# Performance work log

Hardware: AMD Instinct MI355X
Metric: run time of the kernel (lower is better)

Reference implementation:

```python
import jax, jax.numpy as jnp
import numpy as np

B, S, HID = 2, 1024, 4096
NH, NKV, HD = 32, 8, 128
GROUPS = NH // NKV  # 4
BITS = 8
SCALING = HD ** -0.5


def quantize_lastdim(x, bits=BITS):
    """Asymmetric min-max fake-quant per row of the last dim (groupsize=-1),
    matching ActQuantizer.find_params + quantize/dequantize."""
    qmax = float(2 ** bits - 1)
    xmin = jnp.minimum(jnp.min(x, axis=-1, keepdims=True), 0.0)
    xmax = jnp.maximum(jnp.max(x, axis=-1, keepdims=True), 0.0)
    rng = xmax - xmin
    scale = jnp.where(rng == 0, 1.0, rng / qmax)
    zero = jnp.round(-xmin / scale)
    q = jnp.clip(jnp.round(x / scale) + zero, 0.0, qmax)
    return (q - zero) * scale


def rotate_half(x):
    x1, x2 = jnp.split(x, 2, axis=-1)
    return jnp.concatenate([-x2, x1], axis=-1)


def setup_inputs() -> dict:
    key = jax.random.key(0)
    ks = jax.random.split(key, 5)
    hidden_states = jax.random.normal(ks[0], (B, S, HID), dtype=jnp.float32)
    w_std = 0.02
    Wq = w_std * jax.random.normal(ks[1], (NH * HD, HID), dtype=jnp.float32)
    Wk = w_std * jax.random.normal(ks[2], (NKV * HD, HID), dtype=jnp.float32)
    Wv = w_std * jax.random.normal(ks[3], (NKV * HD, HID), dtype=jnp.float32)
    Wo = w_std * jax.random.normal(ks[4], (HID, NH * HD), dtype=jnp.float32)
    # RoPE tables (theta=10000)
    inv_freq = 1.0 / (10000.0 ** (jnp.arange(0, HD, 2, dtype=jnp.float32) / HD))
    freqs = jnp.outer(jnp.arange(S, dtype=jnp.float32), inv_freq)  # [S, HD/2]
    emb = jnp.concatenate([freqs, freqs], axis=-1)  # [S, HD]
    cos = jnp.broadcast_to(jnp.cos(emb)[None], (B, S, HD)).astype(jnp.float32)
    sin = jnp.broadcast_to(jnp.sin(emb)[None], (B, S, HD)).astype(jnp.float32)
    # additive causal mask [B,1,S,S]
    causal = jnp.tril(jnp.ones((S, S), dtype=bool))
    attention_mask = jnp.where(causal, 0.0, -1e9).astype(jnp.float32)
    attention_mask = jnp.broadcast_to(attention_mask[None, None], (B, 1, S, S))
    return {"hidden_states": hidden_states, "cos": cos, "sin": sin,
            "attention_mask": attention_mask, "Wq": Wq, "Wk": Wk, "Wv": Wv, "Wo": Wo}


def reference(hidden_states, cos, sin, attention_mask, Wq, Wk, Wv, Wo):
    b, s, _ = hidden_states.shape
    # projections -> [B, H, S, D]
    q = (hidden_states @ Wq.T).reshape(b, s, NH, HD).transpose(0, 2, 1, 3)
    k = (hidden_states @ Wk.T).reshape(b, s, NKV, HD).transpose(0, 2, 1, 3)
    v = (hidden_states @ Wv.T).reshape(b, s, NKV, HD).transpose(0, 2, 1, 3)
    # RoPE (HF: unsqueeze cos/sin at head dim)
    c = cos[:, None, :, :]
    si = sin[:, None, :, :]
    q = q * c + rotate_half(q) * si
    k = k * c + rotate_half(k) * si
    # SmoothK per-channel: subtract per-channel mean over the sequence
    # (softmax-invariant outlier smoothing of K before quantization)
    k = k - jnp.mean(k, axis=2, keepdims=True)
    # activation fake-quant of Q, K (per token over head_dim)
    q = quantize_lastdim(q)
    k = quantize_lastdim(k)
    # V quantized along the sequence axis (module transposes dims 2,3 first)
    v = quantize_lastdim(v.transpose(0, 1, 3, 2)).transpose(0, 1, 3, 2)
    # GQA repeat
    k_rep = jnp.repeat(k, GROUPS, axis=1)
    v_rep = jnp.repeat(v, GROUPS, axis=1)
    scores = jnp.einsum('bhqd,bhkd->bhqk', q, k_rep) * SCALING + attention_mask
    w = jax.nn.softmax(scores.astype(jnp.float32), axis=-1).astype(q.dtype)
    # fake-quant attention weights per row (groupsize=-1, so no padding)
    w = quantize_lastdim(w)
    attn = jnp.einsum('bhqk,bhkd->bhqd', w, v_rep)
    attn = attn.transpose(0, 2, 1, 3).reshape(b, s, NH * HD)
    out = attn @ Wo.T
    return (out, w)
```

## Files before the change

### kernel.cpp

```cpp
#include <hip/hip_runtime.h>
#include <math.h>
#include <stdint.h>

typedef unsigned int u32;
typedef unsigned short u16;
typedef __bf16 bf16x8 __attribute__((ext_vector_type(8)));
typedef float f32x4 __attribute__((ext_vector_type(4)));
typedef unsigned short u16x8 __attribute__((ext_vector_type(8)));
typedef unsigned short u16x4 __attribute__((ext_vector_type(4)));

constexpr int   Bb  = 2;
constexpr int   Ss  = 1024;
constexpr int   HID = 4096;
constexpr int   NH  = 32;
constexpr int   NKV = 8;
constexpr int   HD  = 128;
constexpr float SCALING = 0.0883883476483184405501f;

enum { M_QKV = 0, M_OUT = 3 };

__device__ __forceinline__ u16 f2bf(float f) {
  u32 u = __builtin_bit_cast(u32, f);
  u = u + 0x7fffu + ((u >> 16) & 1u);
  return (u16)(u >> 16);
}

__device__ __forceinline__ void gld_lds16(const void* g, void* l) {
  __builtin_amdgcn_global_load_lds(
      (const __attribute__((address_space(1))) u32*)(uintptr_t)g,
      (__attribute__((address_space(3))) u32*)(uintptr_t)l, 16, 0, 0);
}

template <int MODE, int NREP>
__global__ __launch_bounds__(512) void mfma_gemm(
    const u16* __restrict__ Abf_g,
    const u16* __restrict__ B0, const u16* __restrict__ B1,
    const u16* __restrict__ B2,
    float* __restrict__ Cf, float* __restrict__ Ck, float* __restrict__ Cv,
    int K) {
  constexpr int BN = NREP * 64;
  constexpr int BCW = BN / 128;
  __shared__ u16 As[4][256 * 32];
  __shared__ u16 Bs[4][BN * 32];

  const int tid = threadIdx.x;
  const int lane = tid & 63;
  const int wid = tid >> 6;
  const int wr = wid >> 2;
  const int wc = wid & 3;

  const int m0 = blockIdx.y * 256;
  int nloc = 0;

  const u16* Abf = Abf_g + (size_t)m0 * K;
  const u16* Bp = nullptr;
  int which = 0;

  if (MODE == M_QKV) {
    const int j = blockIdx.x;
    if (j < 16)      { which = 0; Bp = B0 + (size_t)j * 256 * K;        nloc = j * 256; }
    else if (j < 20) { which = 1; Bp = B1 + (size_t)(j - 16) * 256 * K; nloc = (j - 16) * 256; }
    else             { which = 2; Bp = B2 + (size_t)(j - 20) * 256 * K; nloc = (j - 20) * 256; }
  } else {
    Bp = B0 + (size_t)blockIdx.x * BN * K;
    nloc = blockIdx.x * BN;
  }

  f32x4 acc[8][NREP];
#pragma unroll
  for (int i = 0; i < 8; i++)
#pragma unroll
    for (int j = 0; j < NREP; j++) acc[i][j] = (f32x4){0.f, 0.f, 0.f, 0.f};

  const int fr = lane & 15;
  const int fq = lane >> 4;
  const int srow = lane >> 2;
  const int ssl = lane & 3;

  const int nk = K >> 5;

  auto stage = [&](int t, int sbuf) {
    const int ko = t * 32;
#pragma unroll
    for (int cc = 0; cc < 2; ++cc) {
      const int c = wid * 2 + cc;
      const int r = c * 16 + srow;
      gld_lds16(Abf + (size_t)r * K + ko + ((ssl ^ ((r >> 1) & 3)) * 8),
                &As[sbuf][c * 512]);
    }
#pragma unroll
    for (int cc = 0; cc < BCW; ++cc) {
      const int c = wid * BCW + cc;
      const int r = c * 16 + srow;
      gld_lds16(Bp + (size_t)r * K + ko + ((ssl ^ ((r >> 1) & 3)) * 8),
                &Bs[sbuf][c * 512]);
    }
  };

  stage(0, 0);
  stage(1, 1);
  stage(2, 2);
  if (NREP == 4) { asm volatile("s_waitcnt vmcnt(8)" ::: "memory"); }
  else           { asm volatile("s_waitcnt vmcnt(6)" ::: "memory"); }
  __builtin_amdgcn_sched_barrier(0);
  __builtin_amdgcn_s_barrier();

  for (int kt = 0; kt < nk; ++kt) {
    const int cur = kt & 3;
    if (kt + 3 < nk) stage(kt + 3, (kt + 3) & 3);

    bf16x8 av[8], bv[NREP];
#pragma unroll
    for (int i = 0; i < 8; ++i) {
      const int r = wr * 128 + i * 16 + fr;
      av[i] = *(const bf16x8*)&As[cur][r * 32 + ((fq ^ ((r >> 1) & 3)) * 8)];
    }
#pragma unroll
    for (int j = 0; j < NREP; ++j) {
      const int r = wc * (NREP * 16) + j * 16 + fr;
      bv[j] = *(const bf16x8*)&Bs[cur][r * 32 + ((fq ^ ((r >> 1) & 3)) * 8)];
    }

    __builtin_amdgcn_s_setprio(1);
#pragma unroll
    for (int i = 0; i < 8; i++)
#pragma unroll
      for (int j = 0; j < NREP; j++)
        acc[i][j] = __builtin_amdgcn_mfma_f32_16x16x32_bf16(av[i], bv[j], acc[i][j], 0, 0, 0);
    __builtin_amdgcn_s_setprio(0);

    if (kt + 3 < nk) {
      if (NREP == 4) { asm volatile("s_waitcnt vmcnt(8)" ::: "memory"); }
      else           { asm volatile("s_waitcnt vmcnt(6)" ::: "memory"); }
    } else if (kt + 3 == nk) {
      if (NREP == 4) { asm volatile("s_waitcnt vmcnt(4)" ::: "memory"); }
      else           { asm volatile("s_waitcnt vmcnt(3)" ::: "memory"); }
    } else {
      asm volatile("s_waitcnt vmcnt(0)" ::: "memory");
    }
    __builtin_amdgcn_sched_barrier(0);
    __builtin_amdgcn_s_barrier();
  }

#pragma unroll
  for (int i = 0; i < 8; i++) {
#pragma unroll
    for (int j = 0; j < NREP; j++) {
      const int n = nloc + wc * (NREP * 16) + j * 16 + fr;
#pragma unroll
      for (int e = 0; e < 4; e++) {
        const int m = m0 + wr * 128 + i * 16 + fq * 4 + e;
        float val = acc[i][j][e];
        if (MODE == M_QKV) {
          const int b = m >> 10, s = m & 1023, h = n >> 7, d = n & 127;
          if (which == 0)      Cf[((size_t)(b * NH + h) * Ss + s) * HD + d] = val;
          else if (which == 1) Ck[((size_t)(b * NKV + h) * Ss + s) * HD + d] = val;
          else                 Cv[((size_t)(b * NKV + h) * HD + d) * Ss + s] = val;
        } else {
          Cf[(size_t)m * HID + n] = val;
        }
      }
    }
  }
}

__global__ __launch_bounds__(256) void fused_attn(
    const u16* __restrict__ qb,
    const u16* __restrict__ kb,
    const u16* __restrict__ vTb,
    float* __restrict__ wout,
    u16* __restrict__ attnb) {
  __shared__ u16 Ks[64 * 128];
  __shared__ u16 Vs[128 * 64];
  __shared__ u16 plds[4][16 * 64];
  __shared__ float scl_l[4][16];

  const int a = 15 - (int)(blockIdx.x >> 6);
  const int bh = blockIdx.x & 63;
  const int b = bh >> 5, h = bh & 31;
  const int kv = h >> 2;
  const int tid = threadIdx.x;
  const int lane = tid & 63;
  const int wq = tid >> 6;
  const int fr = lane & 15, fq = lane >> 4;

  const int nt = a + 1;
  const int Q0 = a * 64;
  const int qw0 = Q0 + wq * 16;

  const u16* Kb = kb + (size_t)(b * NKV + kv) * Ss * HD;
  const u16* Vb = vTb + (size_t)(b * NKV + kv) * HD * Ss;
  float* wrow = wout + (size_t)bh * Ss * Ss;

  if (a < 15) {
    const int base = 64 * nt;
    const int n4 = 16 * (15 - a);
#pragma unroll
    for (int r0 = 0; r0 < 4; ++r0) {
      const int row = Q0 + r0 * 16 + (tid >> 4);
      float4* wp = (float4*)&wrow[(size_t)row * Ss + base];
      for (int c = tid & 15; c < n4; c += 16) wp[c] = float4{0.f, 0.f, 0.f, 0.f};
    }
  }

  bf16x8 qf[4];
#pragma unroll
  for (int kk = 0; kk < 4; kk++)
    qf[kk] = *(const bf16x8*)&qb[((size_t)bh * Ss + qw0 + fr) * HD + kk * 32 + fq * 8];

  float m[4], l[4];
#pragma unroll
  for (int i = 0; i < 4; i++) { m[i] = -1e30f; l[i] = 0.f; }

  for (int t = 0; t < nt; ++t) {
    __syncthreads();
#pragma unroll
    for (int c = 0; c < 4; ++c) {
      const int idx0 = (c * 4 + wq) * 64;
      const int idx = idx0 + lane;
      const int row = idx >> 4, sl = idx & 15;
      const int slot = sl ^ (row & 15);
      gld_lds16(Kb + (size_t)(t * 64 + row) * HD + slot * 8, &Ks[idx0 * 8]);
    }
    __syncthreads();

    f32x4 sa[4];
#pragma unroll
    for (int jn = 0; jn < 4; jn++) sa[jn] = (f32x4){0.f, 0.f, 0.f, 0.f};
#pragma unroll
    for (int kk = 0; kk < 4; ++kk) {
      bf16x8 kfv[4];
#pragma unroll
      for (int jn = 0; jn < 4; ++jn) {
        const int row = jn * 16 + fr;
        kfv[jn] = *(const bf16x8*)&Ks[row * 128 + (((kk * 4 + fq) ^ fr) * 8)];
      }
#pragma unroll
      for (int jn = 0; jn < 4; ++jn)
        sa[jn] = __builtin_amdgcn_mfma_f32_16x16x32_bf16(qf[kk], kfv[jn], sa[jn], 0, 0, 0);
    }

    const bool diag = (t == a);
#pragma unroll
    for (int e = 0; e < 4; ++e) {
      const int qrow = qw0 + fq * 4 + e;
      float sv[4];
      float rmax = -1e30f;
#pragma unroll
      for (int jn = 0; jn < 4; ++jn) {
        float s = sa[jn][e] * SCALING;
        if (diag && (t * 64 + jn * 16 + fr > qrow)) s = -1e30f;
        sv[jn] = s;
        rmax = fmaxf(rmax, s);
      }
#pragma unroll
      for (int o = 1; o < 16; o <<= 1) rmax = fmaxf(rmax, __shfl_xor(rmax, o));
      const float mn = fmaxf(m[e], rmax);
      const float cc = __expf(m[e] - mn);
      float rs = __expf(sv[0] - mn) + __expf(sv[1] - mn) +
                 __expf(sv[2] - mn) + __expf(sv[3] - mn);
#pragma unroll
      for (int o = 1; o < 16; o <<= 1) rs += __shfl_xor(rs, o);
      l[e] = l[e] * cc + rs;
      m[e] = mn;
    }
  }

  float scl[4];
#pragma unroll
  for (int e = 0; e < 4; e++) scl[e] = 1.f / (255.f * l[e]);
  if (fr == 0) {
#pragma unroll
    for (int e = 0; e < 4; e++) scl_l[wq][fq * 4 + e] = scl[e];
  }

  f32x4 acc2[8];
#pragma unroll
  for (int j = 0; j < 8; j++) acc2[j] = (f32x4){0.f, 0.f, 0.f, 0.f};

  u16* pl = &plds[wq][0];
  const int wrrow = lane >> 2, wrq = lane & 3;
  const float sclr = scl_l[wq][wrrow];

  for (int t = 0; t < nt; ++t) {
    __syncthreads();
#pragma unroll
    for (int c = 0; c < 4; ++c) {
      const int idx0 = (c * 4 + wq) * 64;
      const int idx = idx0 + lane;
      {
        const int row = idx >> 4, sl = idx & 15;
        const int slot = sl ^ (row & 15);
        gld_lds16(Kb + (size_t)(t * 64 + row) * HD + slot * 8, &Ks[idx0 * 8]);
      }
      {
        const int d = idx >> 3, sl = idx & 7;
        const int slot = sl ^ (d & 7);
        gld_lds16(Vb + (size_t)d * Ss + t * 64 + slot * 8, &Vs[idx0 * 8]);
      }
    }
    __syncthreads();

    f32x4 sa[4];
#pragma unroll
    for (int jn = 0; jn < 4; jn++) sa[jn] = (f32x4){0.f, 0.f, 0.f, 0.f};
#pragma unroll
    for (int kk = 0; kk < 4; ++kk) {
      bf16x8 kfv[4];
#pragma unroll
      for (int jn = 0; jn < 4; ++jn) {
        const int row = jn * 16 + fr;
        kfv[jn] = *(const bf16x8*)&Ks[row * 128 + (((kk * 4 + fq) ^ fr) * 8)];
      }
#pragma unroll
      for (int jn = 0; jn < 4; ++jn)
        sa[jn] = __builtin_amdgcn_mfma_f32_16x16x32_bf16(qf[kk], kfv[jn], sa[jn], 0, 0, 0);
    }

    const bool diag = (t == a);
#pragma unroll
    for (int e = 0; e < 4; ++e) {
      const int qrow = qw0 + fq * 4 + e;
      const int r16 = fq * 4 + e;
#pragma unroll
      for (int jn = 0; jn < 4; ++jn) {
        const int kc = t * 64 + jn * 16 + fr;
        float qv = 0.f;
        if (!diag || kc <= qrow)
          qv = rintf(fminf(255.f * __expf(sa[jn][e] * SCALING - m[e]), 255.f));
        const int col = jn * 16 + fr;
        const int byte = r16 * 128 + (((col >> 3) ^ (r16 & 7)) * 16) + (col & 7) * 2;
        *(u16*)((char*)pl + byte) = f2bf(qv);
      }
    }

    {
      const int s0 = (2 * wrq) ^ (wrrow & 7);
      const int s1 = (2 * wrq + 1) ^ (wrrow & 7);
      bf16x8 p0 = *(const bf16x8*)((char*)pl + wrrow * 128 + s0 * 16);
      bf16x8 p1 = *(const bf16x8*)((char*)pl + wrrow * 128 + s1 * 16);
      float* wp = &wrow[(size_t)(qw0 + wrrow) * Ss + t * 64 + wrq * 16];
      float4 o0, o1, o2, o3;
      o0.x = (float)p0[0] * sclr; o0.y = (float)p0[1] * sclr;
      o0.z = (float)p0[2] * sclr; o0.w = (float)p0[3] * sclr;
      o1.x = (float)p0[4] * sclr; o1.y = (float)p0[5] * sclr;
      o1.z = (float)p0[6] * sclr; o1.w = (float)p0[7] * sclr;
      o2.x = (float)p1[0] * sclr; o2.y = (float)p1[1] * sclr;
      o2.z = (float)p1[2] * sclr; o2.w = (float)p1[3] * sclr;
      o3.x = (float)p1[4] * sclr; o3.y = (float)p1[5] * sclr;
      o3.z = (float)p1[6] * sclr; o3.w = (float)p1[7] * sclr;
      ((float4*)wp)[0] = o0; ((float4*)wp)[1] = o1;
      ((float4*)wp)[2] = o2; ((float4*)wp)[3] = o3;
    }

#pragma unroll
    for (int kk2 = 0; kk2 < 2; ++kk2) {
      const bf16x8 pa = *(const bf16x8*)((char*)pl + fr * 128 + (((kk2 * 4 + fq) ^ (fr & 7)) * 16));
#pragma unroll
      for (int jn2 = 0; jn2 < 8; ++jn2) {
        const int d = jn2 * 16 + fr;
        const bf16x8 vb = *(const bf16x8*)&Vs[d * 64 + (((kk2 * 4 + fq) ^ (d & 7)) * 8)];
        acc2[jn2] = __builtin_amdgcn_mfma_f32_16x16x32_bf16(pa, vb, acc2[jn2], 0, 0, 0);
      }
    }
  }

#pragma unroll
  for (int e = 0; e < 4; ++e) {
    const int qrow = qw0 + fq * 4 + e;
#pragma unroll
    for (int jn2 = 0; jn2 < 8; ++jn2)
      attnb[((size_t)b * Ss + qrow) * HID + h * HD + jn2 * 16 + fr] =
          f2bf(acc2[jn2][e] * scl[e]);
  }
}

constexpr int CB_HS = Bb * Ss * HID / 2048;
constexpr int CB_WQ = NH * HD * HID / 2048;
constexpr int CB_WK = NKV * HD * HID / 2048;
constexpr int CB_WV = CB_WK;
constexpr int CB_WO = HID * NH * HD / 2048;

__global__ __launch_bounds__(256) void convert_all(
    const float* __restrict__ hs, const float* __restrict__ wq,
    const float* __restrict__ wk, const float* __restrict__ wv,
    const float* __restrict__ wo,
    u16* __restrict__ hsb, u16* __restrict__ wqb, u16* __restrict__ wkb,
    u16* __restrict__ wvb, u16* __restrict__ wob) {
  const int bid = blockIdx.x;
  const float* src;
  u16* dst;
  int base;
  if (bid < CB_HS) { src = hs; dst = hsb; base = 0; }
  else if (bid < CB_HS + CB_WQ) { src = wq; dst = wqb; base = CB_HS; }
  else if (bid < CB_HS + CB_WQ + CB_WK) { src = wk; dst = wkb; base = CB_HS + CB_WQ; }
  else if (bid < CB_HS + CB_WQ + CB_WK + CB_WV) { src = wv; dst = wvb; base = CB_HS + CB_WQ + CB_WK; }
  else { src = wo; dst = wob; base = CB_HS + CB_WQ + CB_WK + CB_WV; }
  const int i = (bid - base) * 256 + threadIdx.x;
  float4 a = ((const float4*)src)[2 * i];
  float4 b = ((const float4*)src)[2 * i + 1];
  u16x8 t;
  t[0] = f2bf(a.x); t[1] = f2bf(a.y); t[2] = f2bf(a.z); t[3] = f2bf(a.w);
  t[4] = f2bf(b.x); t[5] = f2bf(b.y); t[6] = f2bf(b.z); t[7] = f2bf(b.w);
  ((u16x8*)dst)[i] = t;
}

__global__ __launch_bounds__(256) void rope_quant_q(const float* __restrict__ q,
                                                    u16* __restrict__ qb,
                                                    const float* __restrict__ cs,
                                                    const float* __restrict__ sn) {
  const int row = blockIdx.x * 4 + (threadIdx.x >> 6);
  const int lane = threadIdx.x & 63;
  const int s = row & (Ss - 1);
  const int b = row >> 15;
  const float* p = q + (size_t)row * HD;
  const float* cp = cs + ((size_t)b * Ss + s) * HD;
  const float* sp = sn + ((size_t)b * Ss + s) * HD;
  float x1 = p[lane], x2 = p[lane + 64];
  float r1 = x1 * cp[lane] - x2 * sp[lane];
  float r2 = x2 * cp[lane + 64] + x1 * sp[lane + 64];
  float mn = fminf(0.f, fminf(r1, r2));
  float mx = fmaxf(0.f, fmaxf(r1, r2));
#pragma unroll
  for (int o = 32; o; o >>= 1) {
    mn = fminf(mn, __shfl_xor(mn, o));
    mx = fmaxf(mx, __shfl_xor(mx, o));
  }
  float rng = mx - mn;
  float scale = (rng == 0.f) ? 1.f : rng / 255.f;
  float zero = rintf(-mn / scale);
  float q1 = fminf(fmaxf(rintf(r1 / scale) + zero, 0.f), 255.f);
  float q2 = fminf(fmaxf(rintf(r2 / scale) + zero, 0.f), 255.f);
  qb[(size_t)row * HD + lane] = f2bf((q1 - zero) * scale);
  qb[(size_t)row * HD + lane + 64] = f2bf((q2 - zero) * scale);
}

__global__ __launch_bounds__(256) void rope_k(float* __restrict__ k,
                                              const float* __restrict__ cs,
                                              const float* __restrict__ sn) {
  const int row = blockIdx.x * 4 + (threadIdx.x >> 6);
  const int lane = threadIdx.x & 63;
  const int s = row & (Ss - 1);
  const int b = row >> 13;
  float* p = k + (size_t)row * HD;
  const float* cp = cs + ((size_t)b * Ss + s) * HD;
  const float* sp = sn + ((size_t)b * Ss + s) * HD;
  float x1 = p[lane], x2 = p[lane + 64];
  float r1 = x1 * cp[lane] - x2 * sp[lane];
  float r2 = x2 * cp[lane + 64] + x1 * sp[lane + 64];
  p[lane] = r1;
  p[lane + 64] = r2;
}

__global__ __launch_bounds__(1024) void kmean_kernel(const float* __restrict__ k,
                                                     float* __restrict__ kmean) {
  const int bh = blockIdx.x;
  const int d = threadIdx.x & 127;
  const int sl = threadIdx.x >> 7;
  const float* p = k + (size_t)bh * Ss * HD;
  float sum = 0.f;
  for (int s = sl; s < Ss; s += 8) sum += p[(size_t)s * HD + d];
  __shared__ float lds[8][128];
  lds[sl][d] = sum;
  __syncthreads();
  if (threadIdx.x < 128) {
    float t = 0.f;
#pragma unroll
    for (int i = 0; i < 8; i++) t += lds[i][threadIdx.x];
    kmean[bh * HD + threadIdx.x] = t * (1.f / 1024.f);
  }
}

__global__ __launch_bounds__(256) void k_subquant(const float* __restrict__ k,
                                                  u16* __restrict__ kb,
                                                  const float* __restrict__ kmean) {
  const int row = blockIdx.x * 4 + (threadIdx.x >> 6);
  const int lane = threadIdx.x & 63;
  const int bh = row >> 10;
  const float* p = k + (size_t)row * HD;
  float x1 = p[lane] - kmean[bh * HD + lane];
  float x2 = p[lane + 64] - kmean[bh * HD + lane + 64];
  float mn = fminf(0.f, fminf(x1, x2));
  float mx = fmaxf(0.f, fmaxf(x1, x2));
#pragma unroll
  for (int o = 32; o; o >>= 1) {
    mn = fminf(mn, __shfl_xor(mn, o));
    mx = fmaxf(mx, __shfl_xor(mx, o));
  }
  float rng = mx - mn;
  float scale = (rng == 0.f) ? 1.f : rng / 255.f;
  float zero = rintf(-mn / scale);
  float q1 = fminf(fmaxf(rintf(x1 / scale) + zero, 0.f), 255.f);
  float q2 = fminf(fmaxf(rintf(x2 / scale) + zero, 0.f), 255.f);
  kb[(size_t)row * HD + lane] = f2bf((q1 - zero) * scale);
  kb[(size_t)row * HD + lane + 64] = f2bf((q2 - zero) * scale);
}

__global__ __launch_bounds__(256) void vquant(const float* __restrict__ vT,
                                              u16* __restrict__ vTb) {
  const float* p = vT + (size_t)blockIdx.x * Ss;
  const int t = threadIdx.x;
  float4 x = ((const float4*)p)[t];
  float mn = fminf(0.f, fminf(fminf(x.x, x.y), fminf(x.z, x.w)));
  float mx = fmaxf(0.f, fmaxf(fmaxf(x.x, x.y), fmaxf(x.z, x.w)));
#pragma unroll
  for (int o = 32; o; o >>= 1) {
    mn = fminf(mn, __shfl_xor(mn, o));
    mx = fmaxf(mx, __shfl_xor(mx, o));
  }
  __shared__ float smn[4], smx[4];
  const int wid = t >> 6, lane = t & 63;
  if (lane == 0) { smn[wid] = mn; smx[wid] = mx; }
  __syncthreads();
  mn = fminf(fminf(smn[0], smn[1]), fminf(smn[2], smn[3]));
  mx = fmaxf(fmaxf(smx[0], smx[1]), fmaxf(smx[2], smx[3]));
  float rng = mx - mn;
  float scale = (rng == 0.f) ? 1.f : rng / 255.f;
  float zero = rintf(-mn / scale);
  u16x4 o4;
  o4[0] = f2bf((fminf(fmaxf(rintf(x.x / scale) + zero, 0.f), 255.f) - zero) * scale);
  o4[1] = f2bf((fminf(fmaxf(rintf(x.y / scale) + zero, 0.f), 255.f) - zero) * scale);
  o4[2] = f2bf((fminf(fmaxf(rintf(x.z / scale) + zero, 0.f), 255.f) - zero) * scale);
  o4[3] = f2bf((fminf(fmaxf(rintf(x.w / scale) + zero, 0.f), 255.f) - zero) * scale);
  ((u16x4*)vTb)[(size_t)blockIdx.x * 256 + t] = o4;
}

extern "C" void kernel_launch(void* const* d_in, const int* in_sizes, int n_in,
                              void* d_out, int out_size, void* d_ws, size_t ws_size,
                              hipStream_t stream) {
  const float* hs = (const float*)d_in[0];
  const float* cosp = (const float*)d_in[1];
  const float* sinp = (const float*)d_in[2];
  const float* Wq = (const float*)d_in[4];
  const float* Wk = (const float*)d_in[5];
  const float* Wv = (const float*)d_in[6];
  const float* Wo = (const float*)d_in[7];

  float* out = (float*)d_out;
  float* wout = out + (size_t)Bb * Ss * HID;

  char* wsp = (char*)d_ws;
  auto alloc = [&](size_t bytes) {
    char* p = wsp;
    wsp += (bytes + 255) & ~(size_t)255;
    return p;
  };
  float* q     = (float*)alloc((size_t)Bb * NH * Ss * HD * 4);
  float* k     = (float*)alloc((size_t)Bb * NKV * Ss * HD * 4);
  float* vT    = (float*)alloc((size_t)Bb * NKV * Ss * HD * 4);
  float* kmean = (float*)alloc((size_t)Bb * NKV * HD * 4);
  u16* hsb = (u16*)alloc((size_t)Bb * Ss * HID * 2);
  u16* qb  = (u16*)alloc((size_t)Bb * NH * Ss * HD * 2);
  u16* kb  = (u16*)alloc((size_t)Bb * NKV * Ss * HD * 2);
  u16* vTb = (u16*)alloc((size_t)Bb * NKV * Ss * HD * 2);
  u16* Wqb = (u16*)alloc((size_t)NH * HD * HID * 2);
  u16* Wkb = (u16*)alloc((size_t)NKV * HD * HID * 2);
  u16* Wvb = (u16*)alloc((size_t)NKV * HD * HID * 2);
  u16* Wob = (u16*)alloc((size_t)HID * NH * HD * 2);
  u16* attnb = (u16*)q;

  convert_all<<<CB_HS + CB_WQ + CB_WK + CB_WV + CB_WO, 256, 0, stream>>>(
      hs, Wq, Wk, Wv, Wo, hsb, Wqb, Wkb, Wvb, Wob);

  mfma_gemm<M_QKV, 4><<<dim3(24, 8), 512, 0, stream>>>(
      hsb, Wqb, Wkb, Wvb, q, k, vT, HID);

  rope_quant_q<<<(Bb * NH * Ss) / 4, 256, 0, stream>>>(q, qb, cosp, sinp);
  rope_k<<<(Bb * NKV * Ss) / 4, 256, 0, stream>>>(k, cosp, sinp);
  kmean_kernel<<<Bb * NKV, 1024, 0, stream>>>(k, kmean);
  k_subquant<<<(Bb * NKV * Ss) / 4, 256, 0, stream>>>(k, kb, kmean);
  vquant<<<Bb * NKV * HD, 256, 0, stream>>>(vT, vTb);

  fused_attn<<<dim3(1024), 256, 0, stream>>>(qb, kb, vTb, wout, attnb);

  mfma_gemm<M_OUT, 2><<<dim3(32, 8), 512, 0, stream>>>(
      attnb, Wob, nullptr, nullptr, out, nullptr, nullptr, HID);
}
```

Measured before the change: 446.6 us.

## Restructure GEMM to 128x256 tiles with BK=64 and triple buffering

Rewrites the bf16 MFMA GEMM used for the QKV and output projections. Block tiles change from 256xBN with BK=32 and four LDS stages to 128x256 with BK=64 and three stages, using a new 8-way XOR swizzle. The loads for the next stage are split across two half-K MFMA phases so they overlap compute. Grids change to 24x16 and 16x16, which gives more blocks for CU occupancy at the cost of less A reuse per block and extra barriers per iteration.

```diff
diff --git a/kernel.cpp b/kernel.cpp
--- a/kernel.cpp
+++ b/kernel.cpp
@@ -31,25 +31,25 @@
       (__attribute__((address_space(3))) u32*)(uintptr_t)l, 16, 0, 0);
 }
 
-template <int MODE, int NREP>
+template <int MODE>
 __global__ __launch_bounds__(512) void mfma_gemm(
     const u16* __restrict__ Abf_g,
     const u16* __restrict__ B0, const u16* __restrict__ B1,
     const u16* __restrict__ B2,
     float* __restrict__ Cf, float* __restrict__ Ck, float* __restrict__ Cv,
     int K) {
-  constexpr int BN = NREP * 64;
-  constexpr int BCW = BN / 128;
-  __shared__ u16 As[4][256 * 32];
-  __shared__ u16 Bs[4][BN * 32];
+  __shared__ u16 As[3][128 * 64];
+  __shared__ u16 Bs[3][256 * 64];
 
   const int tid = threadIdx.x;
   const int lane = tid & 63;
   const int wid = tid >> 6;
   const int wr = wid >> 2;
   const int wc = wid & 3;
-
-  const int m0 = blockIdx.y * 256;
+  const int fr = lane & 15;
+  const int fq = lane >> 4;
+
+  const int m0 = blockIdx.y * 128;
   int nloc = 0;
 
   const u16* Abf = Abf_g + (size_t)m0 * K;
@@ -62,94 +62,123 @@
     else if (j < 20) { which = 1; Bp = B1 + (size_t)(j - 16) * 256 * K; nloc = (j - 16) * 256; }
     else             { which = 2; Bp = B2 + (size_t)(j - 20) * 256 * K; nloc = (j - 20) * 256; }
   } else {
-    Bp = B0 + (size_t)blockIdx.x * BN * K;
-    nloc = blockIdx.x * BN;
-  }
-
-  f32x4 acc[8][NREP];
-#pragma unroll
-  for (int i = 0; i < 8; i++)
-#pragma unroll
-    for (int j = 0; j < NREP; j++) acc[i][j] = (f32x4){0.f, 0.f, 0.f, 0.f};
-
-  const int fr = lane & 15;
-  const int fq = lane >> 4;
-  const int srow = lane >> 2;
-  const int ssl = lane & 3;
-
-  const int nk = K >> 5;
-
-  auto stage = [&](int t, int sbuf) {
-    const int ko = t * 32;
-#pragma unroll
-    for (int cc = 0; cc < 2; ++cc) {
-      const int c = wid * 2 + cc;
-      const int r = c * 16 + srow;
-      gld_lds16(Abf + (size_t)r * K + ko + ((ssl ^ ((r >> 1) & 3)) * 8),
-                &As[sbuf][c * 512]);
-    }
-#pragma unroll
-    for (int cc = 0; cc < BCW; ++cc) {
-      const int c = wid * BCW + cc;
-      const int r = c * 16 + srow;
-      gld_lds16(Bp + (size_t)r * K + ko + ((ssl ^ ((r >> 1) & 3)) * 8),
-                &Bs[sbuf][c * 512]);
+    Bp = B0 + (size_t)blockIdx.x * 256 * K;
+    nloc = blockIdx.x * 256;
+  }
+
+  f32x4 acc[4][4];
+#pragma unroll
+  for (int i = 0; i < 4; i++)
+#pragma unroll
+    for (int j = 0; j < 4; j++) acc[i][j] = (f32x4){0.f, 0.f, 0.f, 0.f};
+
+  const int arow0 = wr * 64 + wc * 16;
+  const int brow0 = wc * 64 + wr * 32;
+  const int sub8 = lane >> 3;
+  const int sl8 = lane & 7;
+
+  auto stageA = [&](int t, int s) {
+    const int ko = t * 64;
+#pragma unroll
+    for (int g = 0; g < 2; ++g) {
+      const int r0 = arow0 + g * 8;
+      const int row = r0 + sub8;
+      gld_lds16(Abf + (size_t)row * K + ko + ((sl8 ^ (row & 7)) * 8),
+                &As[s][r0 * 64]);
     }
   };
-
-  stage(0, 0);
-  stage(1, 1);
-  stage(2, 2);
-  if (NREP == 4) { asm volatile("s_waitcnt vmcnt(8)" ::: "memory"); }
-  else           { asm volatile("s_waitcnt vmcnt(6)" ::: "memory"); }
+  auto stageB2 = [&](int t, int s, int gbase) {
+    const int ko = t * 64;
+#pragma unroll
+    for (int g = 0; g < 2; ++g) {
+      const int r0 = brow0 + (gbase + g) * 8;
+      const int row = r0 + sub8;
+      gld_lds16(Bp + (size_t)row * K + ko + ((sl8 ^ (row & 7)) * 8),
+                &Bs[s][r0 * 64]);
+    }
+  };
+
+  const int nk = K >> 6;
+
+  stageA(0, 0); stageB2(0, 0, 0); stageB2(0, 0, 2);
+  stageA(1, 1); stageB2(1, 1, 0); stageB2(1, 1, 2);
+  asm volatile("s_waitcnt vmcnt(6)" ::: "memory");
   __builtin_amdgcn_sched_barrier(0);
   __builtin_amdgcn_s_barrier();
 
+  int buf = 0, nxt = 2;
   for (int kt = 0; kt < nk; ++kt) {
-    const int cur = kt & 3;
-    if (kt + 3 < nk) stage(kt + 3, (kt + 3) & 3);
-
-    bf16x8 av[8], bv[NREP];
-#pragma unroll
-    for (int i = 0; i < 8; ++i) {
-      const int r = wr * 128 + i * 16 + fr;
-      av[i] = *(const bf16x8*)&As[cur][r * 32 + ((fq ^ ((r >> 1) & 3)) * 8)];
-    }
-#pragma unroll
-    for (int j = 0; j < NREP; ++j) {
-      const int r = wc * (NREP * 16) + j * 16 + fr;
-      bv[j] = *(const bf16x8*)&Bs[cur][r * 32 + ((fq ^ ((r >> 1) & 3)) * 8)];
-    }
-
-    __builtin_amdgcn_s_setprio(1);
-#pragma unroll
-    for (int i = 0; i < 8; i++)
-#pragma unroll
-      for (int j = 0; j < NREP; j++)
-        acc[i][j] = __builtin_amdgcn_mfma_f32_16x16x32_bf16(av[i], bv[j], acc[i][j], 0, 0, 0);
-    __builtin_amdgcn_s_setprio(0);
-
-    if (kt + 3 < nk) {
-      if (NREP == 4) { asm volatile("s_waitcnt vmcnt(8)" ::: "memory"); }
-      else           { asm volatile("s_waitcnt vmcnt(6)" ::: "memory"); }
-    } else if (kt + 3 == nk) {
-      if (NREP == 4) { asm volatile("s_waitcnt vmcnt(4)" ::: "memory"); }
-      else           { asm volatile("s_waitcnt vmcnt(3)" ::: "memory"); }
+    const bool st = (kt + 2 < nk);
+
+    {
+      bf16x8 av[4], bv[4];
+#pragma unroll
+      for (int i = 0; i < 4; ++i) {
+        const int r = wr * 64 + i * 16 + fr;
+        av[i] = *(const bf16x8*)&As[buf][r * 64 + ((fq ^ (r & 7)) * 8)];
+      }
+#pragma unroll
+      for (int j = 0; j < 4; ++j) {
+        const int r = wc * 64 + j * 16 + fr;
+        bv[j] = *(const bf16x8*)&Bs[buf][r * 64 + ((fq ^ (r & 7)) * 8)];
+      }
+      if (st) { stageA(kt + 2, nxt); stageB2(kt + 2, nxt, 0); }
+      __builtin_amdgcn_s_barrier();
+      asm volatile("s_waitcnt lgkmcnt(0)" ::: "memory");
+      __builtin_amdgcn_sched_barrier(0);
+      __builtin_amdgcn_s_setprio(1);
+#pragma unroll
+      for (int i = 0; i < 4; i++)
+#pragma unroll
+        for (int j = 0; j < 4; j++)
+          acc[i][j] = __builtin_amdgcn_mfma_f32_16x16x32_bf16(av[i], bv[j], acc[i][j], 0, 0, 0);
+      __builtin_amdgcn_s_setprio(0);
+    }
+
+    {
+      bf16x8 av[4], bv[4];
+#pragma unroll
+      for (int i = 0; i < 4; ++i) {
+        const int r = wr * 64 + i * 16 + fr;
+        av[i] = *(const bf16x8*)&As[buf][r * 64 + (((4 + fq) ^ (r & 7)) * 8)];
+      }
+#pragma unroll
+      for (int j = 0; j < 4; ++j) {
+        const int r = wc * 64 + j * 16 + fr;
+        bv[j] = *(const bf16x8*)&Bs[buf][r * 64 + (((4 + fq) ^ (r & 7)) * 8)];
+      }
+      if (st) { stageB2(kt + 2, nxt, 2); }
+      __builtin_amdgcn_s_barrier();
+      asm volatile("s_waitcnt lgkmcnt(0)" ::: "memory");
+      __builtin_amdgcn_sched_barrier(0);
+      __builtin_amdgcn_s_setprio(1);
+#pragma unroll
+      for (int i = 0; i < 4; i++)
+#pragma unroll
+        for (int j = 0; j < 4; j++)
+          acc[i][j] = __builtin_amdgcn_mfma_f32_16x16x32_bf16(av[i], bv[j], acc[i][j], 0, 0, 0);
+      __builtin_amdgcn_s_setprio(0);
+    }
+
+    if (st) {
+      asm volatile("s_waitcnt vmcnt(6)" ::: "memory");
     } else {
       asm volatile("s_waitcnt vmcnt(0)" ::: "memory");
     }
     __builtin_amdgcn_sched_barrier(0);
     __builtin_amdgcn_s_barrier();
-  }
-
-#pragma unroll
-  for (int i = 0; i < 8; i++) {
-#pragma unroll
-    for (int j = 0; j < NREP; j++) {
-      const int n = nloc + wc * (NREP * 16) + j * 16 + fr;
+    buf = (buf == 2) ? 0 : buf + 1;
+    nxt = (nxt == 2) ? 0 : nxt + 1;
+  }
+
+#pragma unroll
+  for (int i = 0; i < 4; i++) {
+#pragma unroll
+    for (int j = 0; j < 4; j++) {
+      const int n = nloc + wc * 64 + j * 16 + fr;
 #pragma unroll
       for (int e = 0; e < 4; e++) {
-        const int m = m0 + wr * 128 + i * 16 + fq * 4 + e;
+        const int m = m0 + wr * 64 + i * 16 + fq * 4 + e;
         float val = acc[i][j][e];
         if (MODE == M_QKV) {
           const int b = m >> 10, s = m & 1023, h = n >> 7, d = n & 127;
@@ -562,7 +591,7 @@
   convert_all<<<CB_HS + CB_WQ + CB_WK + CB_WV + CB_WO, 256, 0, stream>>>(
       hs, Wq, Wk, Wv, Wo, hsb, Wqb, Wkb, Wvb, Wob);
 
-  mfma_gemm<M_QKV, 4><<<dim3(24, 8), 512, 0, stream>>>(
+  mfma_gemm<M_QKV><<<dim3(24, 16), 512, 0, stream>>>(
       hsb, Wqb, Wkb, Wvb, q, k, vT, HID);
 
   rope_quant_q<<<(Bb * NH * Ss) / 4, 256, 0, stream>>>(q, qb, cosp, sinp);
@@ -573,6 +602,6 @@
 
   fused_attn<<<dim3(1024), 256, 0, stream>>>(qb, kb, vTb, wout, attnb);
 
-  mfma_gemm<M_OUT, 2><<<dim3(32, 8), 512, 0, stream>>>(
+  mfma_gemm<M_OUT><<<dim3(16, 16), 512, 0, stream>>>(
       attnb, Wob, nullptr, nullptr, out, nullptr, nullptr, HID);
 }
```

New measurement: 442.0 us. About the same (-1.0%).
